# Kernel optimization log

Hardware: AMD Instinct MI355X
Metric: run time of the kernel (lower is better)

Reference implementation:

```python
import jax, jax.numpy as jnp
import numpy as np

H = 128
GATE_CODES = (2, 3, 4, 1)  # order in original forward: NOT, AND, OR, MAJ


def gru_step(x, h, Wih, bih, Whh, bhh):
    # single-step PyTorch GRU math; weights stored transposed [H, 3H]
    gi = x @ Wih + bih
    gh = h @ Whh + bhh
    ir, iz, inn = jnp.split(gi, 3, axis=-1)
    hr, hz, hn = jnp.split(gh, 3, axis=-1)
    r = jax.nn.sigmoid(ir + hr)
    z = jax.nn.sigmoid(iz + hz)
    n = jnp.tanh(inn + r * hn)
    return (1.0 - z) * n + z * h


def setup_inputs() -> dict:
    key = jax.random.key(0)
    N, E, L = 60000, 180000, 3
    ks = jax.random.split(key, 16)

    def p(k, shape, fan_in):
        return (jax.random.normal(k, shape, jnp.float32) / np.float32(np.sqrt(fan_in)))

    return dict(
        gate=jax.random.randint(ks[0], (N,), 0, 6),
        edge_index=jax.random.randint(ks[1], (2, E), 0, N),
        forward_level=jax.random.randint(ks[2], (N,), 0, L),
        num_levels=L,
        Ws_self=p(ks[3], (6, H), 6), Ws_nbr=p(ks[4], (6, H), 6),
        Wt_self=p(ks[5], (6, H), 6), Wt_nbr=p(ks[6], (6, H), 6),
        hs_W=p(ks[7], (2 * H, H), 2 * H), hs_b=jnp.zeros((H,), jnp.float32),
        aggr_W1=p(ks[8], (4, 2 * H, H), 2 * H), aggr_b1=jnp.zeros((4, H), jnp.float32),
        aggr_W2=p(ks[9], (4, H, H), H), aggr_b2=jnp.zeros((4, H), jnp.float32),
        gru_Wih=p(ks[10], (4, H, 3 * H), H), gru_bih=jnp.zeros((4, 3 * H), jnp.float32),
        gru_Whh=p(ks[11], (4, H, 3 * H), H), gru_bhh=jnp.zeros((4, 3 * H), jnp.float32),
    )


def reference(gate, edge_index, forward_level, num_levels,
              Ws_self, Ws_nbr, Wt_self, Wt_nbr, hs_W, hs_b,
              aggr_W1, aggr_b1, aggr_W2, aggr_b2,
              gru_Wih, gru_bih, gru_Whh, gru_bhh):
    N = gate.shape[0]
    src, dst = edge_index[0], edge_index[1]

    # struct encoder: one-hop MP producing source/target embeddings s, t [N, H]
    one_hot = jax.nn.one_hot(gate, 6, dtype=jnp.float32)
    nbr_in = jax.ops.segment_sum(one_hot[src], dst, num_segments=N)
    nbr_out = jax.ops.segment_sum(one_hot[dst], src, num_segments=N)
    s = jax.nn.relu(one_hot @ Ws_self + nbr_in @ Ws_nbr)
    t = jax.nn.relu(one_hot @ Wt_self + nbr_out @ Wt_nbr)

    hs = jnp.concatenate([s, t], -1) @ hs_W + hs_b          # [N, H]
    hf = jnp.zeros((N, H), jnp.float32)

    gate_dst = gate[dst]
    lvl_dst = forward_level[dst]
    # num_rounds = 1; levels 1..num_levels-1, gate types disjoint per node
    for level in range(1, num_levels):
        node_state = jnp.concatenate([hs, hf], -1)           # [N, 2H]
        src_state = node_state[src]                          # [E, 2H] gather
        for gi, code in enumerate(GATE_CODES):
            emask = ((gate_dst == code) & (lvl_dst == level)).astype(jnp.float32)[:, None]
            msg = jax.nn.relu(src_state @ aggr_W1[gi] + aggr_b1[gi]) @ aggr_W2[gi] + aggr_b2[gi]
            agg = jax.ops.segment_sum(msg * emask, dst, num_segments=N)  # scatter-add
            h_new = gru_step(agg, hf, gru_Wih[gi], gru_bih[gi], gru_Whh[gi], gru_bhh[gi])
            nmask = ((gate == code) & (forward_level == level))[:, None]
            hf = jnp.where(nmask, h_new, hf)
    return hs, hf
```

## Files before the change

kernel.cpp:

```cpp
#include <hip/hip_runtime.h>

#define H 128

typedef __bf16 bf16x8 __attribute__((ext_vector_type(8)));
typedef __bf16 bf16x4 __attribute__((ext_vector_type(4)));
typedef float  f32x4  __attribute__((ext_vector_type(4)));

__device__ __forceinline__ int gate_to_gi(int g) {
    switch (g) {
        case 2: return 0;
        case 3: return 1;
        case 4: return 2;
        case 1: return 3;
        default: return -1;
    }
}

__global__ __launch_bounds__(256)
void zero_ws(f32x4* __restrict__ p, int n16) {
    int i = blockIdx.x * blockDim.x + threadIdx.x;
    f32x4 z = {};
    for (; i < n16; i += gridDim.x * blockDim.x) p[i] = z;
}

#define BB_CHUNK 512
#define BB_IT (BB_CHUNK / 256)
__global__ __launch_bounds__(256)
void bucket_build(const int* __restrict__ gate, const int* __restrict__ ei,
                  const int* __restrict__ lvl, int E, int N,
                  int* __restrict__ ncnt, int* __restrict__ nbuf, int ncap,
                  int* __restrict__ cnt_in, int* __restrict__ cnt_out) {
    __shared__ int lcnt[8];
    __shared__ int lbase[8];
    const int tid = threadIdx.x;
    const int total = max(E, N);

    for (int chunk = blockIdx.x * BB_CHUNK; chunk < total; chunk += gridDim.x * BB_CHUNK) {
        if (tid < 8) lcnt[tid] = 0;
        __syncthreads();
        int nbkt[BB_IT], npos[BB_IT];
        #pragma unroll
        for (int it = 0; it < BB_IT; ++it) {
            int i = chunk + it * 256 + tid;
            nbkt[it] = -1;
            if (i < E) {
                int s = ei[i], d = ei[E + i];
                atomicAdd(&cnt_in[d * 6 + gate[s]], 1);
                atomicAdd(&cnt_out[s * 6 + gate[d]], 1);
            }
            if (i < N) {
                int gi = gate_to_gi(gate[i]);
                int L = lvl[i];
                if (gi >= 0 && L >= 1 && L <= 2) {
                    int b = (L - 1) * 4 + gi;
                    nbkt[it] = b;
                    npos[it] = atomicAdd(&lcnt[b], 1);
                }
            }
        }
        __syncthreads();
        if (tid < 8) lbase[tid] = atomicAdd(&ncnt[tid], lcnt[tid]);
        __syncthreads();
        #pragma unroll
        for (int it = 0; it < BB_IT; ++it) {
            int i = chunk + it * 256 + tid;
            if (nbkt[it] >= 0) {
                int p = lbase[nbkt[it]] + npos[it];
                if (p < ncap) nbuf[nbkt[it] * ncap + p] = i;
            }
        }
        __syncthreads();
    }
}

__global__ __launch_bounds__(256)
void node_alloc(const int* __restrict__ gate, const int* __restrict__ lvl,
                const int* __restrict__ cnt_in, int N, int ecap,
                int* __restrict__ galloc, int* __restrict__ cursor) {
    __shared__ int lcnt[8];
    __shared__ int lbase[8];
    const int tid = threadIdx.x;
    for (int base = blockIdx.x * 256; base < N; base += gridDim.x * 256) {
        if (tid < 8) lcnt[tid] = 0;
        __syncthreads();
        int n = base + tid;
        int b = -1, local = 0;
        if (n < N) {
            int gi = gate_to_gi(gate[n]);
            int L = lvl[n];
            if (gi >= 0 && L >= 1 && L <= 2) {
                b = (L - 1) * 4 + gi;
                int deg = 0;
                #pragma unroll
                for (int c = 0; c < 6; ++c) deg += cnt_in[n * 6 + c];
                local = atomicAdd(&lcnt[b], deg);
            }
        }
        __syncthreads();
        if (tid < 8) lbase[tid] = atomicAdd(&galloc[tid], lcnt[tid]);
        __syncthreads();
        if (b >= 0) cursor[n] = b * ecap + lbase[b] + local;
        __syncthreads();
    }
}

__global__ __launch_bounds__(256)
void edge_scatter(const int* __restrict__ gate, const int* __restrict__ ei,
                  const int* __restrict__ lvl, int E,
                  int* __restrict__ cursor, int2* __restrict__ elist) {
    int e = blockIdx.x * blockDim.x + threadIdx.x;
    if (e >= E) return;
    int d = ei[E + e];
    int gi = gate_to_gi(gate[d]);
    if (gi < 0) return;
    int L = lvl[d];
    if (L < 1 || L > 2) return;
    int slot = atomicAdd(&cursor[d], 1);
    elist[slot] = make_int2(ei[e], d);
}

__global__ __launch_bounds__(256)
void prep_weights(const float* __restrict__ aW1, const float* __restrict__ aW2,
                  const float* __restrict__ gWih, const float* __restrict__ hsW,
                  __bf16* __restrict__ W1T, __bf16* __restrict__ W2T,
                  __bf16* __restrict__ WihT, __bf16* __restrict__ hsWT) {
    int z = blockIdx.z;
    const float* src;
    __bf16* dst;
    int K, C;
    if (z < 4)       { src = aW1 + (size_t)z * 256 * 128;       dst = W1T + (size_t)z * 128 * 256; K = 256; C = 128; }
    else if (z < 8)  { src = aW2 + (size_t)(z - 4) * 128 * 128; dst = W2T + (size_t)(z - 4) * 128 * 128; K = 128; C = 128; }
    else if (z < 12) { src = gWih + (size_t)(z - 8) * 128 * 384; dst = WihT + (size_t)(z - 8) * 384 * 128; K = 128; C = 384; }
    else             { src = hsW;                                dst = hsWT;                        K = 256; C = 128; }
    __shared__ float tile[32][33];
    const int tilesC = C >> 5;
    const int ntile = (K >> 5) * tilesC;
    const int t = blockIdx.x;
    if (t >= ntile) return;
    const int k0 = (t / tilesC) << 5;
    const int c0 = (t % tilesC) << 5;
    const int tid = threadIdx.x;
    #pragma unroll
    for (int e = 0; e < 4; ++e) {
        int pos = e * 256 + tid;
        int kk = pos >> 5, cc = pos & 31;
        tile[kk][cc] = src[(size_t)(k0 + kk) * C + c0 + cc];
    }
    __syncthreads();
    #pragma unroll
    for (int e = 0; e < 4; ++e) {
        int pos = e * 256 + tid;
        int cc = pos >> 5, kk = pos & 31;
        dst[(size_t)(c0 + cc) * K + k0 + kk] = (__bf16)tile[kk][cc];
    }
}

__global__ __launch_bounds__(256, 2)
void encoder_mfma(const int* __restrict__ gate, const int* __restrict__ lvl,
                  const int* __restrict__ cnt_in, const int* __restrict__ cnt_out,
                  const float* __restrict__ Ws_self, const float* __restrict__ Ws_nbr,
                  const float* __restrict__ Wt_self, const float* __restrict__ Wt_nbr,
                  const __bf16* __restrict__ hsWT, const float* __restrict__ hs_b,
                  float* __restrict__ out, __bf16* __restrict__ mir,
                  float* __restrict__ agg, int N) {
    __shared__ __bf16 st[16][264];
    const int tid = threadIdx.x;
    const int lane = tid & 63;
    const int w = tid >> 6;
    const int row = tid >> 4;
    const int c0 = (tid & 15) * 8;

    bf16x8 bw[8][2];
    #pragma unroll
    for (int kk = 0; kk < 8; ++kk)
        #pragma unroll
        for (int j = 0; j < 2; ++j) {
            int col = w * 32 + j * 16 + (lane & 15);
            bw[kk][j] = *(const bf16x8*)&hsWT[(size_t)col * 256 + kk * 32 + (lane >> 4) * 8];
        }
    float hbc[2];
    #pragma unroll
    for (int j = 0; j < 2; ++j) hbc[j] = hs_b[w * 32 + j * 16 + (lane & 15)];

    const int ntiles = (N + 15) >> 4;
    for (int t = blockIdx.x; t < ntiles; t += gridDim.x) {
        const int base = t * 16;
        int n = base + row;
        if (n >= N) n = N - 1;
        const int g = gate[n];
        const int L = lvl[n];
        int cin[6], cout[6];
        #pragma unroll
        for (int k = 0; k < 6; ++k) { cin[k] = cnt_in[n * 6 + k]; cout[k] = cnt_out[n * 6 + k]; }
        f32x4 s0 = *(const f32x4*)&Ws_self[g * H + c0];
        f32x4 s1 = *(const f32x4*)&Ws_self[g * H + c0 + 4];
        f32x4 t0 = *(const f32x4*)&Wt_self[g * H + c0];
        f32x4 t1 = *(const f32x4*)&Wt_self[g * H + c0 + 4];
        #pragma unroll
        for (int k = 0; k < 6; ++k) {
            float ci = (float)cin[k], co = (float)cout[k];
            s0 += ci * *(const f32x4*)&Ws_nbr[k * H + c0];
            s1 += ci * *(const f32x4*)&Ws_nbr[k * H + c0 + 4];
            t0 += co * *(const f32x4*)&Wt_nbr[k * H + c0];
            t1 += co * *(const f32x4*)&Wt_nbr[k * H + c0 + 4];
        }
        bf16x8 ps, pt;
        #pragma unroll
        for (int j = 0; j < 4; ++j) {
            ps[j]     = (__bf16)fmaxf(s0[j], 0.f);
            ps[4 + j] = (__bf16)fmaxf(s1[j], 0.f);
            pt[j]     = (__bf16)fmaxf(t0[j], 0.f);
            pt[4 + j] = (__bf16)fmaxf(t1[j], 0.f);
        }
        *(bf16x8*)&st[row][c0]       = ps;
        *(bf16x8*)&st[row][128 + c0] = pt;
        if (base + row < N) {
            f32x4 z = {};
            const bool bucketed = (gate_to_gi(g) >= 0 && L >= 1 && L <= 2);
            if (bucketed) {
                *(f32x4*)&agg[(size_t)n * H + c0]     = z;
                *(f32x4*)&agg[(size_t)n * H + c0 + 4] = z;
            } else {
                *(f32x4*)&out[(size_t)N * H + (size_t)n * H + c0]     = z;
                *(f32x4*)&out[(size_t)N * H + (size_t)n * H + c0 + 4] = z;
            }
        }
        __syncthreads();
        f32x4 acc[2] = {};
        #pragma unroll
        for (int kk = 0; kk < 8; ++kk) {
            bf16x8 a = *(const bf16x8*)&st[lane & 15][kk * 32 + (lane >> 4) * 8];
            #pragma unroll
            for (int j = 0; j < 2; ++j)
                acc[j] = __builtin_amdgcn_mfma_f32_16x16x32_bf16(a, bw[kk][j], acc[j], 0, 0, 0);
        }
        #pragma unroll
        for (int j = 0; j < 2; ++j) {
            int col = w * 32 + j * 16 + (lane & 15);
            #pragma unroll
            for (int r = 0; r < 4; ++r) {
                int nn = base + (lane >> 4) * 4 + r;
                if (nn < N) {
                    float v = acc[j][r] + hbc[j];
                    out[(size_t)nn * H + col] = v;
                    mir[(size_t)nn * 256 + col] = (__bf16)v;
                    mir[(size_t)nn * 256 + 128 + col] = (__bf16)0.f;
                }
            }
        }
        __syncthreads();
    }
}

template<int KHALF>
__global__ __launch_bounds__(256, 2)
void edge_msg_seg(int level, const int* __restrict__ etot,
                  const int2* __restrict__ elist, int ecap,
                  const __bf16* __restrict__ W1T, const __bf16* __restrict__ W2T,
                  const float* __restrict__ b1, const float* __restrict__ b2,
                  const __bf16* __restrict__ mir, float* __restrict__ agg) {
    const int gi = blockIdx.y;
    const int b = (level - 1) * 4 + gi;
    const int ecnt = etot[b];
    const int ntiles = (ecnt + 15) >> 4;
    if (ntiles == 0) return;

    __shared__ __bf16 st[16][264];
    __shared__ __bf16 hid[16][136];
    __shared__ float msgbuf[16][132];
    __shared__ int ssrc[16], sdst[16];
    __shared__ int leadrow[17];
    __shared__ int nlead;

    const int tid = threadIdx.x;
    const int lane = tid & 63;
    const int w = tid >> 6;
    const __bf16* w1 = W1T + (size_t)gi * 128 * 256;
    const __bf16* w2 = W2T + (size_t)gi * 128 * 128;

    bf16x8 w1f[KHALF][2], w2f[4][2];
    #pragma unroll
    for (int kk = 0; kk < KHALF; ++kk)
        #pragma unroll
        for (int j = 0; j < 2; ++j) {
            int col = w * 32 + j * 16 + (lane & 15);
            w1f[kk][j] = *(const bf16x8*)&w1[(size_t)col * 256 + kk * 32 + (lane >> 4) * 8];
        }
    #pragma unroll
    for (int kk = 0; kk < 4; ++kk)
        #pragma unroll
        for (int j = 0; j < 2; ++j) {
            int col = w * 32 + j * 16 + (lane & 15);
            w2f[kk][j] = *(const bf16x8*)&w2[(size_t)col * 128 + kk * 32 + (lane >> 4) * 8];
        }
    float b1c[2], b2c[2];
    #pragma unroll
    for (int j = 0; j < 2; ++j) {
        int col = w * 32 + j * 16 + (lane & 15);
        b1c[j] = b1[gi * H + col];
        b2c[j] = b2[gi * H + col];
    }

    for (int t = blockIdx.x; t < ntiles; t += gridDim.x) {
        const int base = t * 16;
        const int rem = min(16, ecnt - base);
        if (tid < 64) {
            if (tid < 16) {
                int2 e = elist[b * ecap + base + min(tid, rem - 1)];
                ssrc[tid] = e.x;
                sdst[tid] = e.y;
            }
            bool flag = (tid < rem) && (tid == 0 || sdst[tid] != sdst[tid - 1]);
            unsigned long long m = __ballot(flag);
            if (flag) {
                int rank = __popcll(m & ((1ull << tid) - 1));
                leadrow[rank] = tid;
            }
            if (tid == 0) {
                int nl = __popcll(m);
                nlead = nl;
                leadrow[nl] = rem;
            }
        }
        __syncthreads();
        #pragma unroll
        for (int rep = 0; rep < KHALF / 4; ++rep) {
            int idx = rep * 256 + tid;
            int r = idx / (KHALF * 4);
            int c = idx - r * (KHALF * 4);
            *(bf16x8*)&st[r][c * 8] = *(const bf16x8*)&mir[(size_t)ssrc[r] * 256 + c * 8];
        }
        __syncthreads();
        f32x4 acc[2] = {};
        #pragma unroll
        for (int kk = 0; kk < KHALF; ++kk) {
            bf16x8 a = *(const bf16x8*)&st[lane & 15][kk * 32 + (lane >> 4) * 8];
            #pragma unroll
            for (int j = 0; j < 2; ++j)
                acc[j] = __builtin_amdgcn_mfma_f32_16x16x32_bf16(a, w1f[kk][j], acc[j], 0, 0, 0);
        }
        #pragma unroll
        for (int j = 0; j < 2; ++j) {
            int col = w * 32 + j * 16 + (lane & 15);
            #pragma unroll
            for (int r = 0; r < 4; ++r)
                hid[(lane >> 4) * 4 + r][col] = (__bf16)fmaxf(acc[j][r] + b1c[j], 0.f);
        }
        __syncthreads();
        f32x4 acc2[2] = {};
        #pragma unroll
        for (int kk = 0; kk < 4; ++kk) {
            bf16x8 a = *(const bf16x8*)&hid[lane & 15][kk * 32 + (lane >> 4) * 8];
            #pragma unroll
            for (int j = 0; j < 2; ++j)
                acc2[j] = __builtin_amdgcn_mfma_f32_16x16x32_bf16(a, w2f[kk][j], acc2[j], 0, 0, 0);
        }
        #pragma unroll
        for (int j = 0; j < 2; ++j) {
            int col = w * 32 + j * 16 + (lane & 15);
            #pragma unroll
            for (int r = 0; r < 4; ++r)
                msgbuf[(lane >> 4) * 4 + r][col] = acc2[j][r] + b2c[j];
        }
        __syncthreads();
        const int nl = nlead;
        for (int idx = tid; idx < (nl << 7); idx += 256) {
            int li = idx >> 7, c = idx & 127;
            int r0 = leadrow[li], r1 = leadrow[li + 1];
            float s = msgbuf[r0][c];
            for (int r = r0 + 1; r < r1; ++r) s += msgbuf[r][c];
            atomicAdd(&agg[(size_t)sdst[r0] * H + c], s);
        }
        __syncthreads();
    }
}

__global__ __launch_bounds__(256, 2)
void gru_mfma(const int* __restrict__ ncnt, const int* __restrict__ nbuf, int ncap,
              int level, int N,
              const __bf16* __restrict__ WihT, const float* __restrict__ bih,
              const float* __restrict__ bhh,
              const float* __restrict__ agg, float* __restrict__ out,
              __bf16* __restrict__ mir) {
    const int gi = blockIdx.y;
    const int bucket = (level - 1) * 4 + gi;
    const int cnt = min(ncnt[bucket], ncap);
    const int ntiles = (cnt + 15) >> 4;
    if (ntiles == 0) return;

    __shared__ __bf16 x[16][136];
    __shared__ int nid[16];
    const int tid = threadIdx.x;
    const int lane = tid & 63;
    const int w = tid >> 6;
    const __bf16* wih = WihT + (size_t)gi * 384 * 128;

    bf16x8 wf[4][3][2];
    #pragma unroll
    for (int kk = 0; kk < 4; ++kk)
        #pragma unroll
        for (int p = 0; p < 3; ++p)
            #pragma unroll
            for (int j = 0; j < 2; ++j) {
                int oc = p * 128 + w * 32 + j * 16 + (lane & 15);
                wf[kk][p][j] = *(const bf16x8*)&wih[(size_t)oc * 128 + kk * 32 + (lane >> 4) * 8];
            }
    float bir[2], biz[2], bin[2], bhn[2];
    #pragma unroll
    for (int j = 0; j < 2; ++j) {
        int col = w * 32 + j * 16 + (lane & 15);
        bir[j] = bih[gi * 384 + col] + bhh[gi * 384 + col];
        biz[j] = bih[gi * 384 + 128 + col] + bhh[gi * 384 + 128 + col];
        bin[j] = bih[gi * 384 + 256 + col];
        bhn[j] = bhh[gi * 384 + 256 + col];
    }

    for (int t = blockIdx.x; t < ntiles; t += gridDim.x) {
        const int base = t * 16;
        const int rem = min(16, cnt - base);
        if (tid < 16) nid[tid] = nbuf[bucket * ncap + base + min(tid, rem - 1)];
        __syncthreads();
        #pragma unroll
        for (int rep = 0; rep < 2; ++rep) {
            int idx = rep * 256 + tid;
            int row = idx >> 5, c4 = idx & 31;
            f32x4 v = *(const f32x4*)&agg[(size_t)nid[row] * H + c4 * 4];
            bf16x4 p;
            p[0] = (__bf16)v[0]; p[1] = (__bf16)v[1]; p[2] = (__bf16)v[2]; p[3] = (__bf16)v[3];
            *(bf16x4*)&x[row][c4 * 4] = p;
        }
        __syncthreads();
        f32x4 acc[3][2] = {};
        #pragma unroll
        for (int kk = 0; kk < 4; ++kk) {
            bf16x8 a = *(const bf16x8*)&x[lane & 15][kk * 32 + (lane >> 4) * 8];
            #pragma unroll
            for (int p = 0; p < 3; ++p)
                #pragma unroll
                for (int j = 0; j < 2; ++j)
                    acc[p][j] = __builtin_amdgcn_mfma_f32_16x16x32_bf16(a, wf[kk][p][j], acc[p][j], 0, 0, 0);
        }
        #pragma unroll
        for (int j = 0; j < 2; ++j) {
            int col = w * 32 + j * 16 + (lane & 15);
            #pragma unroll
            for (int r = 0; r < 4; ++r) {
                int row = (lane >> 4) * 4 + r;
                if (row >= rem) continue;
                float rr = 1.f / (1.f + expf(-(acc[0][j][r] + bir[j])));
                float zz = 1.f / (1.f + expf(-(acc[1][j][r] + biz[j])));
                float nn = tanhf(acc[2][j][r] + bin[j] + rr * bhn[j]);
                float h = (1.f - zz) * nn;
                out[(size_t)N * H + (size_t)nid[row] * H + col] = h;
                mir[(size_t)nid[row] * 256 + 128 + col] = (__bf16)h;
            }
        }
        __syncthreads();
    }
}

extern "C" void kernel_launch(void* const* d_in, const int* in_sizes, int n_in,
                              void* d_out, int out_size, void* d_ws, size_t ws_size,
                              hipStream_t stream) {
    const int*   gate    = (const int*)d_in[0];
    const int*   ei      = (const int*)d_in[1];
    const int*   lvl     = (const int*)d_in[2];
    const float* Ws_self = (const float*)d_in[4];
    const float* Ws_nbr  = (const float*)d_in[5];
    const float* Wt_self = (const float*)d_in[6];
    const float* Wt_nbr  = (const float*)d_in[7];
    const float* hs_W    = (const float*)d_in[8];
    const float* hs_b    = (const float*)d_in[9];
    const float* aW1     = (const float*)d_in[10];
    const float* ab1     = (const float*)d_in[11];
    const float* aW2     = (const float*)d_in[12];
    const float* ab2     = (const float*)d_in[13];
    const float* gWih    = (const float*)d_in[14];
    const float* gbih    = (const float*)d_in[15];
    const float* gbhh    = (const float*)d_in[17];

    const int N = in_sizes[0];
    const int E = in_sizes[1] / 2;
    const int ECAP = ((E / 4) + 15) & ~15;
    const int NCAP = ((N / 4) + 15) & ~15;

    char* wsb = (char*)d_ws;
    size_t off = 0;
    float* agg = (float*)(wsb + off);         off += (size_t)N * H * sizeof(float);
    const size_t zstart = off;
    int* cnt_in = (int*)(wsb + off);          off += (size_t)N * 6 * sizeof(int);
    int* cnt_out = (int*)(wsb + off);         off += (size_t)N * 6 * sizeof(int);
    int* ncnt = (int*)(wsb + off);            off += 8 * sizeof(int);
    int* galloc = (int*)(wsb + off);          off += 8 * sizeof(int); off = (off + 63) & ~(size_t)63;
    const size_t zero_bytes = off - zstart;
    int* cursor = (int*)(wsb + off);          off += (size_t)N * sizeof(int); off = (off + 7) & ~(size_t)7;
    int2* elist = (int2*)(wsb + off);         off += (size_t)8 * ECAP * sizeof(int2);
    int* nbuf   = (int*)(wsb + off);          off += (size_t)8 * NCAP * sizeof(int);
    __bf16* mir = (__bf16*)(wsb + off);       off += (size_t)N * 256 * sizeof(__bf16);
    __bf16* W1T = (__bf16*)(wsb + off);       off += (size_t)4 * 128 * 256 * 2;
    __bf16* W2T = (__bf16*)(wsb + off);       off += (size_t)4 * 128 * 128 * 2;
    __bf16* WihT = (__bf16*)(wsb + off);      off += (size_t)4 * 384 * 128 * 2;
    __bf16* hsWT = (__bf16*)(wsb + off);      off += (size_t)128 * 256 * 2;

    float* out = (float*)d_out;

    {
        int n16 = (int)(zero_bytes / 16);
        int blocks = min((n16 + 255) / 256, 2048);
        zero_ws<<<blocks, 256, 0, stream>>>((f32x4*)(wsb + zstart), n16);
    }
    prep_weights<<<dim3(48, 1, 13), 256, 0, stream>>>(aW1, aW2, gWih, hs_W, W1T, W2T, WihT, hsWT);
    const int nchunks = (max(E, N) + BB_CHUNK - 1) / BB_CHUNK;
    bucket_build<<<nchunks, 256, 0, stream>>>(
        gate, ei, lvl, E, N, ncnt, nbuf, NCAP, cnt_in, cnt_out);
    node_alloc<<<(N + 255) / 256, 256, 0, stream>>>(gate, lvl, cnt_in, N, ECAP, galloc, cursor);
    edge_scatter<<<(E + 255) / 256, 256, 0, stream>>>(gate, ei, lvl, E, cursor, elist);
    encoder_mfma<<<512, 256, 0, stream>>>(
        gate, lvl, cnt_in, cnt_out, Ws_self, Ws_nbr, Wt_self, Wt_nbr, hsWT, hs_b,
        out, mir, agg, N);

    edge_msg_seg<4><<<dim3(128, 4), 256, 0, stream>>>(
        1, galloc, elist, ECAP, W1T, W2T, ab1, ab2, mir, agg);
    gru_mfma<<<dim3(64, 4), 256, 0, stream>>>(
        ncnt, nbuf, NCAP, 1, N, WihT, gbih, gbhh, agg, out, mir);
    edge_msg_seg<8><<<dim3(128, 4), 256, 0, stream>>>(
        2, galloc, elist, ECAP, W1T, W2T, ab1, ab2, mir, agg);
    gru_mfma<<<dim3(64, 4), 256, 0, stream>>>(
        ncnt, nbuf, NCAP, 2, N, WihT, gbih, gbhh, agg, out, mir);
}
```

Baseline: 138.2 us.

## Fold zeroing into weight prep, split histogram, and use sentinel cursors in edge scatter

Zeroing the workspace is folded into the prep_weights launch as an extra z-slice, which removes one kernel launch. The old bucket_build is split so that a pure edge histogram kernel runs first and node bucketing moves into node_alloc. edge_scatter now skips its gate and level lookups by relying on a negative sentinel cursor for non-bucketed nodes. The encoder writes the zero half of the bf16 mirror as a vector store instead of scalar stores, and the GRU grid is doubled to raise parallelism. The sentinel scheme depends on atomic increments never bringing the cursor back up to a non-negative value.

```diff
diff --git a/kernel.cpp b/kernel.cpp
--- a/kernel.cpp
+++ b/kernel.cpp
@@ -1,10 +1,13 @@
 #include <hip/hip_runtime.h>
+#include <limits.h>
 
 #define H 128
 
 typedef __bf16 bf16x8 __attribute__((ext_vector_type(8)));
 typedef __bf16 bf16x4 __attribute__((ext_vector_type(4)));
 typedef float  f32x4  __attribute__((ext_vector_type(4)));
+
+#define CUR_SENTINEL (INT_MIN / 2)
 
 __device__ __forceinline__ int gate_to_gi(int g) {
     switch (g) {
@@ -17,114 +20,18 @@
 }
 
 __global__ __launch_bounds__(256)
-void zero_ws(f32x4* __restrict__ p, int n16) {
-    int i = blockIdx.x * blockDim.x + threadIdx.x;
-    f32x4 z = {};
-    for (; i < n16; i += gridDim.x * blockDim.x) p[i] = z;
-}
-
-#define BB_CHUNK 512
-#define BB_IT (BB_CHUNK / 256)
-__global__ __launch_bounds__(256)
-void bucket_build(const int* __restrict__ gate, const int* __restrict__ ei,
-                  const int* __restrict__ lvl, int E, int N,
-                  int* __restrict__ ncnt, int* __restrict__ nbuf, int ncap,
-                  int* __restrict__ cnt_in, int* __restrict__ cnt_out) {
-    __shared__ int lcnt[8];
-    __shared__ int lbase[8];
-    const int tid = threadIdx.x;
-    const int total = max(E, N);
-
-    for (int chunk = blockIdx.x * BB_CHUNK; chunk < total; chunk += gridDim.x * BB_CHUNK) {
-        if (tid < 8) lcnt[tid] = 0;
-        __syncthreads();
-        int nbkt[BB_IT], npos[BB_IT];
-        #pragma unroll
-        for (int it = 0; it < BB_IT; ++it) {
-            int i = chunk + it * 256 + tid;
-            nbkt[it] = -1;
-            if (i < E) {
-                int s = ei[i], d = ei[E + i];
-                atomicAdd(&cnt_in[d * 6 + gate[s]], 1);
-                atomicAdd(&cnt_out[s * 6 + gate[d]], 1);
-            }
-            if (i < N) {
-                int gi = gate_to_gi(gate[i]);
-                int L = lvl[i];
-                if (gi >= 0 && L >= 1 && L <= 2) {
-                    int b = (L - 1) * 4 + gi;
-                    nbkt[it] = b;
-                    npos[it] = atomicAdd(&lcnt[b], 1);
-                }
-            }
-        }
-        __syncthreads();
-        if (tid < 8) lbase[tid] = atomicAdd(&ncnt[tid], lcnt[tid]);
-        __syncthreads();
-        #pragma unroll
-        for (int it = 0; it < BB_IT; ++it) {
-            int i = chunk + it * 256 + tid;
-            if (nbkt[it] >= 0) {
-                int p = lbase[nbkt[it]] + npos[it];
-                if (p < ncap) nbuf[nbkt[it] * ncap + p] = i;
-            }
-        }
-        __syncthreads();
-    }
-}
-
-__global__ __launch_bounds__(256)
-void node_alloc(const int* __restrict__ gate, const int* __restrict__ lvl,
-                const int* __restrict__ cnt_in, int N, int ecap,
-                int* __restrict__ galloc, int* __restrict__ cursor) {
-    __shared__ int lcnt[8];
-    __shared__ int lbase[8];
-    const int tid = threadIdx.x;
-    for (int base = blockIdx.x * 256; base < N; base += gridDim.x * 256) {
-        if (tid < 8) lcnt[tid] = 0;
-        __syncthreads();
-        int n = base + tid;
-        int b = -1, local = 0;
-        if (n < N) {
-            int gi = gate_to_gi(gate[n]);
-            int L = lvl[n];
-            if (gi >= 0 && L >= 1 && L <= 2) {
-                b = (L - 1) * 4 + gi;
-                int deg = 0;
-                #pragma unroll
-                for (int c = 0; c < 6; ++c) deg += cnt_in[n * 6 + c];
-                local = atomicAdd(&lcnt[b], deg);
-            }
-        }
-        __syncthreads();
-        if (tid < 8) lbase[tid] = atomicAdd(&galloc[tid], lcnt[tid]);
-        __syncthreads();
-        if (b >= 0) cursor[n] = b * ecap + lbase[b] + local;
-        __syncthreads();
-    }
-}
-
-__global__ __launch_bounds__(256)
-void edge_scatter(const int* __restrict__ gate, const int* __restrict__ ei,
-                  const int* __restrict__ lvl, int E,
-                  int* __restrict__ cursor, int2* __restrict__ elist) {
-    int e = blockIdx.x * blockDim.x + threadIdx.x;
-    if (e >= E) return;
-    int d = ei[E + e];
-    int gi = gate_to_gi(gate[d]);
-    if (gi < 0) return;
-    int L = lvl[d];
-    if (L < 1 || L > 2) return;
-    int slot = atomicAdd(&cursor[d], 1);
-    elist[slot] = make_int2(ei[e], d);
-}
-
-__global__ __launch_bounds__(256)
 void prep_weights(const float* __restrict__ aW1, const float* __restrict__ aW2,
                   const float* __restrict__ gWih, const float* __restrict__ hsW,
                   __bf16* __restrict__ W1T, __bf16* __restrict__ W2T,
-                  __bf16* __restrict__ WihT, __bf16* __restrict__ hsWT) {
-    int z = blockIdx.z;
+                  __bf16* __restrict__ WihT, __bf16* __restrict__ hsWT,
+                  f32x4* __restrict__ zbase, int zn16) {
+    const int z = blockIdx.z;
+    const int tid = threadIdx.x;
+    if (z == 14) {
+        f32x4 zero = {};
+        for (int i = blockIdx.x * 256 + tid; i < zn16; i += gridDim.x * 256) zbase[i] = zero;
+        return;
+    }
     const float* src;
     __bf16* dst;
     int K, C;
@@ -139,7 +46,6 @@
     if (t >= ntile) return;
     const int k0 = (t / tilesC) << 5;
     const int c0 = (t % tilesC) << 5;
-    const int tid = threadIdx.x;
     #pragma unroll
     for (int e = 0; e < 4; ++e) {
         int pos = e * 256 + tid;
@@ -153,6 +59,68 @@
         int cc = pos >> 5, kk = pos & 31;
         dst[(size_t)(c0 + cc) * K + k0 + kk] = (__bf16)tile[kk][cc];
     }
+}
+
+__global__ __launch_bounds__(256)
+void hist_kernel(const int* __restrict__ gate, const int* __restrict__ ei, int E,
+                 int* __restrict__ cnt_in, int* __restrict__ cnt_out) {
+    int e = blockIdx.x * blockDim.x + threadIdx.x;
+    if (e >= E) return;
+    int s = ei[e], d = ei[E + e];
+    atomicAdd(&cnt_in[d * 6 + gate[s]], 1);
+    atomicAdd(&cnt_out[s * 6 + gate[d]], 1);
+}
+
+__global__ __launch_bounds__(256)
+void node_alloc(const int* __restrict__ gate, const int* __restrict__ lvl,
+                const int* __restrict__ cnt_in, int N, int ecap, int ncap,
+                int* __restrict__ galloc, int* __restrict__ ncnt,
+                int* __restrict__ cursor, int* __restrict__ nbuf) {
+    __shared__ int lcnt[16];
+    __shared__ int lbase[16];
+    const int tid = threadIdx.x;
+    for (int base = blockIdx.x * 256; base < N; base += gridDim.x * 256) {
+        if (tid < 16) lcnt[tid] = 0;
+        __syncthreads();
+        int n = base + tid;
+        int b = -1, local = 0, nlocal = 0;
+        if (n < N) {
+            int gi = gate_to_gi(gate[n]);
+            int L = lvl[n];
+            if (gi >= 0 && L >= 1 && L <= 2) {
+                b = (L - 1) * 4 + gi;
+                int deg = 0;
+                #pragma unroll
+                for (int c = 0; c < 6; ++c) deg += cnt_in[n * 6 + c];
+                local = atomicAdd(&lcnt[b], deg);
+                nlocal = atomicAdd(&lcnt[8 + b], 1);
+            }
+        }
+        __syncthreads();
+        if (tid < 8)       lbase[tid] = atomicAdd(&galloc[tid], lcnt[tid]);
+        else if (tid < 16) lbase[tid] = atomicAdd(&ncnt[tid - 8], lcnt[tid]);
+        __syncthreads();
+        if (n < N) {
+            if (b >= 0) {
+                cursor[n] = b * ecap + lbase[b] + local;
+                int p = lbase[8 + b] + nlocal;
+                if (p < ncap) nbuf[b * ncap + p] = n;
+            } else {
+                cursor[n] = CUR_SENTINEL;
+            }
+        }
+        __syncthreads();
+    }
+}
+
+__global__ __launch_bounds__(256)
+void edge_scatter(const int* __restrict__ ei, int E,
+                  int* __restrict__ cursor, int2* __restrict__ elist) {
+    int e = blockIdx.x * blockDim.x + threadIdx.x;
+    if (e >= E) return;
+    int d = ei[E + e];
+    int slot = atomicAdd(&cursor[d], 1);
+    if (slot >= 0) elist[slot] = make_int2(ei[e], d);
 }
 
 __global__ __launch_bounds__(256, 2)
@@ -216,6 +184,8 @@
         *(bf16x8*)&st[row][128 + c0] = pt;
         if (base + row < N) {
             f32x4 z = {};
+            bf16x8 zb = {};
+            *(bf16x8*)&mir[(size_t)n * 256 + 128 + c0] = zb;
             const bool bucketed = (gate_to_gi(g) >= 0 && L >= 1 && L <= 2);
             if (bucketed) {
                 *(f32x4*)&agg[(size_t)n * H + c0]     = z;
@@ -244,7 +214,6 @@
                     float v = acc[j][r] + hbc[j];
                     out[(size_t)nn * H + col] = v;
                     mir[(size_t)nn * 256 + col] = (__bf16)v;
-                    mir[(size_t)nn * 256 + 128 + col] = (__bf16)0.f;
                 }
             }
         }
@@ -504,27 +473,23 @@
 
     float* out = (float*)d_out;
 
-    {
-        int n16 = (int)(zero_bytes / 16);
-        int blocks = min((n16 + 255) / 256, 2048);
-        zero_ws<<<blocks, 256, 0, stream>>>((f32x4*)(wsb + zstart), n16);
-    }
-    prep_weights<<<dim3(48, 1, 13), 256, 0, stream>>>(aW1, aW2, gWih, hs_W, W1T, W2T, WihT, hsWT);
-    const int nchunks = (max(E, N) + BB_CHUNK - 1) / BB_CHUNK;
-    bucket_build<<<nchunks, 256, 0, stream>>>(
-        gate, ei, lvl, E, N, ncnt, nbuf, NCAP, cnt_in, cnt_out);
-    node_alloc<<<(N + 255) / 256, 256, 0, stream>>>(gate, lvl, cnt_in, N, ECAP, galloc, cursor);
-    edge_scatter<<<(E + 255) / 256, 256, 0, stream>>>(gate, ei, lvl, E, cursor, elist);
+    prep_weights<<<dim3(48, 1, 15), 256, 0, stream>>>(
+        aW1, aW2, gWih, hs_W, W1T, W2T, WihT, hsWT,
+        (f32x4*)(wsb + zstart), (int)(zero_bytes / 16));
+    hist_kernel<<<(E + 255) / 256, 256, 0, stream>>>(gate, ei, E, cnt_in, cnt_out);
+    node_alloc<<<(N + 255) / 256, 256, 0, stream>>>(
+        gate, lvl, cnt_in, N, ECAP, NCAP, galloc, ncnt, cursor, nbuf);
+    edge_scatter<<<(E + 255) / 256, 256, 0, stream>>>(ei, E, cursor, elist);
     encoder_mfma<<<512, 256, 0, stream>>>(
         gate, lvl, cnt_in, cnt_out, Ws_self, Ws_nbr, Wt_self, Wt_nbr, hsWT, hs_b,
         out, mir, agg, N);
 
     edge_msg_seg<4><<<dim3(128, 4), 256, 0, stream>>>(
         1, galloc, elist, ECAP, W1T, W2T, ab1, ab2, mir, agg);
-    gru_mfma<<<dim3(64, 4), 256, 0, stream>>>(
+    gru_mfma<<<dim3(128, 4), 256, 0, stream>>>(
         ncnt, nbuf, NCAP, 1, N, WihT, gbih, gbhh, agg, out, mir);
     edge_msg_seg<8><<<dim3(128, 4), 256, 0, stream>>>(
         2, galloc, elist, ECAP, W1T, W2T, ab1, ab2, mir, agg);
-    gru_mfma<<<dim3(64, 4), 256, 0, stream>>>(
+    gru_mfma<<<dim3(128, 4), 256, 0, stream>>>(
         ncnt, nbuf, NCAP, 2, N, WihT, gbih, gbhh, agg, out, mir);
 }
```

Result: faster. 131.3 us (-5.0%).
